# Optimization experiments

Measured on AMD Instinct MI355X. Metric: run time of the kernel, lower is better.

Reference implementation:

```python
import jax, jax.numpy as jnp
import numpy as np

# Dims (match init_kwargs / input_specs)
B, N, DIM, HEADS, DHEAD, CHUNK = 1, 2048, 1024, 8, 128, 64
HID = 4 * DHEAD            # MemoryMLP expansion_factor=4.0
DI = HEADS * DHEAD         # dim_inner
EPS = 1e-6
MAX_LR = 1.0               # default_step_transform_max_lr


def rmsnorm(x, w):
    return x * jax.lax.rsqrt(jnp.mean(jnp.square(x), -1, keepdims=True) + EPS) * w


def mem_forward(w0, w1, g, x):
    # ResidualNorm(MemoryMLP): y = RMSNorm(gelu(x@w0)@w1)*g + x
    h = jax.nn.gelu(x @ w0, approximate=False) @ w1
    return rmsnorm(h, g) + x


def setup_inputs() -> dict:
    key = jax.random.key(0)
    ks = jax.random.split(key, 12)
    s = lambda i, shape, sc: jax.random.normal(ks[i], shape, jnp.float32) * sc
    return dict(
        x=s(0, (B, N, DIM), 1.0),
        store_norm_w=jnp.ones((DIM,), jnp.float32),
        ret_norm_w=jnp.ones((DIM,), jnp.float32),
        Wq=s(1, (DIM, DI), DIM ** -0.5),
        Wk=s(2, (DIM, DI), DIM ** -0.5),
        Wv=s(3, (DIM, DI), DIM ** -0.5),
        W_step=s(4, (DIM, HEADS), DIM ** -0.5), b_step=jnp.zeros((HEADS,), jnp.float32),
        W_mom=s(5, (DIM, HEADS), DIM ** -0.5), b_mom=jnp.zeros((HEADS,), jnp.float32),
        W_decay=s(6, (DIM, HEADS), DIM ** -0.5), b_decay=jnp.zeros((HEADS,), jnp.float32),
        gate_W=s(7, (DIM, HEADS), DIM ** -0.5),
        combine_W=s(8, (DI, DIM), DI ** -0.5),
        mem_w0=s(9, (HEADS, DHEAD, HID), DHEAD ** -0.5),
        mem_w1=s(10, (HEADS, HID, DHEAD), HID ** -0.5),
        mem_g=jnp.ones((HEADS, DHEAD), jnp.float32),
    )


def reference(x, store_norm_w, ret_norm_w, Wq, Wk, Wv, W_step, b_step,
              W_mom, b_mom, W_decay, b_decay, gate_W, combine_W,
              mem_w0, mem_w1, mem_g):
    b, n, _ = x.shape
    nc = n // CHUNK
    BH = b * HEADS

    # ---- store path ----
    s = rmsnorm(x, store_norm_w)                                 # b n dim
    lr = jax.nn.sigmoid(s @ W_step + b_step) * MAX_LR            # b n h (per-token adaptive step)
    pooled = s.reshape(b, nc, CHUNK, DIM).mean(2)                # b nc dim (AveragePool chunk rep)
    mom = jax.nn.sigmoid(pooled @ W_mom + b_mom)                 # b nc h
    dec = jax.nn.sigmoid(pooled @ W_decay + b_decay)             # b nc h

    def to_chunks(t):  # b n (h d) -> (b h) nc c d
        return t.reshape(b, nc, CHUNK, HEADS, DHEAD).transpose(0, 3, 1, 2, 4).reshape(BH, nc, CHUNK, DHEAD)

    k = to_chunks(s @ Wk)
    v = to_chunks(s @ Wv)
    lr_c = lr.reshape(b, nc, CHUNK, HEADS).transpose(0, 3, 1, 2).reshape(BH, nc, CHUNK)
    mom_bh = mom.transpose(0, 2, 1).reshape(BH, nc)
    dec_bh = dec.transpose(0, 2, 1).reshape(BH, nc)

    # init fast weights per (b h)  (per_head_learned_parameters=True)
    w0 = jnp.broadcast_to(mem_w0[None], (b, HEADS, DHEAD, HID)).reshape(BH, DHEAD, HID)
    w1 = jnp.broadcast_to(mem_w1[None], (b, HEADS, HID, DHEAD)).reshape(BH, HID, DHEAD)
    g = jnp.broadcast_to(mem_g[None], (b, HEADS, DHEAD)).reshape(BH, DHEAD)

    def chunk_loss(w0_, w1_, g_, kc, vc, lrc):
        pred = mem_forward(w0_, w1_, g_, kc)                     # c d
        return jnp.sum(jnp.mean(jnp.square(pred - vc), -1) * lrc)

    grad_chunk = jax.grad(chunk_loss, argnums=(0, 1, 2))
    # vmap over chunks (same weights per chunk, per-sample grads), then over (b h)
    grads = jax.vmap(jax.vmap(grad_chunk, in_axes=(None, None, None, 0, 0, 0)))(w0, w1, g, k, v, lr_c)
    surprises = tuple(-gr for gr in grads)                       # each (BH, nc, ...)

    def combine(a, c):
        ga, xa = a
        gb, xb = c
        return (ga * gb, gb * xa + xb)

    def lin_scan(gates, xs):
        # y_i = gates_i * y_{i-1} + xs_i over chunk axis (axis=1)
        return jax.lax.associative_scan(combine, (gates, xs), axis=1)

    def expand(gates, ref):
        return gates.reshape(gates.shape + (1,) * (ref.ndim - 2))

    # momentum scan per parameter tensor
    updates = tuple(lin_scan(expand(mom_bh, su), su)[1] for su in surprises)

    # weight update scan: W_i = (1 - decay_i) * W_{i-1} + momentum_i, W_{-1} = init
    per_chunk_weights = []
    for upd, w_init in zip(updates, (w0, w1, g)):
        gates = expand(1.0 - dec_bh, upd)
        cumg, y = lin_scan(gates, upd)
        w_seq = y + cumg * w_init[:, None]                       # (BH, nc, ...)
        # retrieval at chunk i uses weights updated through chunk i-1
        per_chunk_weights.append(jnp.concatenate([w_init[:, None], w_seq[:, :-1]], axis=1))
    w0_c, w1_c, g_c = per_chunk_weights

    # ---- retrieve path ----
    r = rmsnorm(x, ret_norm_w)
    q = to_chunks(r @ Wq)                                        # (BH, nc, c, d)
    pred = jax.vmap(jax.vmap(mem_forward))(w0_c, w1_c, g_c, q)   # (BH, nc, c, d)
    out = pred.reshape(b, HEADS, n, DHEAD)                       # b h n d
    gate = jax.nn.sigmoid(r @ gate_W)                            # b n h (retrieve_gate, heads>1)
    out = out * gate.transpose(0, 2, 1)[..., None]
    out = out.transpose(0, 2, 1, 3).reshape(b, n, DI) @ combine_W
    return out
```

## Files before the change

kernel.cpp:

```cpp
#include <hip/hip_runtime.h>
#include <hip/hip_bf16.h>
#include <math.h>

#define NH   8
#define DHD  128
#define HIDN 512
#define CHK  64
#define NCH  32
#define MB   1048576ull

typedef unsigned short u16;
typedef unsigned int   u32;
typedef short s16x8 __attribute__((ext_vector_type(8)));
typedef float f32x4 __attribute__((ext_vector_type(4)));

#define MFMA(a,b,c) __builtin_amdgcn_mfma_f32_16x16x32_bf16((a),(b),(c),0,0,0)

__device__ __forceinline__ float bf2f(u16 v){ return __uint_as_float(((u32)v) << 16); }
__device__ __forceinline__ u16 f2bf(float f){
  u32 u = __float_as_uint(f);
  u += 0x7fffu + ((u >> 16) & 1u);
  return (u16)(u >> 16);
}
__device__ __forceinline__ u32 pack2(float a, float b){
  return (u32)f2bf(a) | ((u32)f2bf(b) << 16);
}
__device__ __forceinline__ float dot2(u32 a, u32 b){
  return __uint_as_float(a << 16)*__uint_as_float(b << 16)
       + __uint_as_float(a & 0xffff0000u)*__uint_as_float(b & 0xffff0000u);
}
__device__ __forceinline__ float waveRedSum(float v){
  #pragma unroll
  for (int off = 32; off; off >>= 1) v += __shfl_xor(v, off);
  return v;
}
__device__ __forceinline__ void gload16(const void* g, void* l){
  __builtin_amdgcn_global_load_lds(
      (const __attribute__((address_space(1))) u32*)g,
      (__attribute__((address_space(3))) u32*)l, 16, 0, 0);
}
__device__ __forceinline__ int swzb(int row, int colb){ return colb ^ ((row & 7) << 4); }
__device__ __forceinline__ int swza(int row, int colb){
  return colb ^ ((row & 7) << 4) ^ (((row >> 3) & 3) << 5);
}



__global__ __launch_bounds__(256) void k_rmsnorm(const float* __restrict__ x,
    const float* __restrict__ wst, const float* __restrict__ wrt,
    u16* __restrict__ s_bf, u16* __restrict__ r_bf){
  int row = blockIdx.x, t = threadIdx.x;
  float4 v = ((const float4*)(x + (size_t)row*1024))[t];
  float ss = v.x*v.x + v.y*v.y + v.z*v.z + v.w*v.w;
  ss = waveRedSum(ss);
  __shared__ float red[4];
  int wv = t >> 6, ln = t & 63;
  if (ln == 0) red[wv] = ss;
  __syncthreads();
  float rr = rsqrtf((red[0]+red[1]+red[2]+red[3])*(1.f/1024.f) + 1e-6f);
  float4 a = ((const float4*)wst)[t];
  float4 b = ((const float4*)wrt)[t];
  uint2 so = make_uint2(pack2(v.x*rr*a.x, v.y*rr*a.y), pack2(v.z*rr*a.z, v.w*rr*a.w));
  uint2 ro = make_uint2(pack2(v.x*rr*b.x, v.y*rr*b.y), pack2(v.z*rr*b.z, v.w*rr*b.w));
  *(uint2*)(s_bf + (size_t)row*1024 + t*4) = so;
  *(uint2*)(r_bf + (size_t)row*1024 + t*4) = ro;
}

__global__ __launch_bounds__(256) void k_pool(const u16* __restrict__ s_bf, float* __restrict__ pooled){
  int c = blockIdx.x; int d = blockIdx.y*256 + threadIdx.x;
  float acc = 0.f;
  for (int tt = 0; tt < 64; ++tt) acc += bf2f(s_bf[((size_t)c*64+tt)*1024 + d]);
  pooled[(size_t)c*1024 + d] = acc * (1.f/64.f);
}

__global__ __launch_bounds__(256) void k_lrgate(const u16* __restrict__ s_bf, const u16* __restrict__ r_bf,
    const u16* __restrict__ WsgL, const float* __restrict__ bstep,
    float* __restrict__ lrc, float* __restrict__ gate){
  int wv = threadIdx.x >> 6, ln = threadIdx.x & 63;
  int tok = blockIdx.x*4 + wv;
  const u16* sp = s_bf + (size_t)tok*1024 + ln*16;
  const u16* rp = r_bf + (size_t)tok*1024 + ln*16;
  uint4 s0 = *(const uint4*)sp, s1 = *(const uint4*)(sp+8);
  uint4 r0 = *(const uint4*)rp, r1 = *(const uint4*)(rp+8);
  #pragma unroll 4
  for (int o = 0; o < 16; ++o){
    const u16* wp = WsgL + (size_t)o*1024 + ln*16;
    uint4 w0v = *(const uint4*)wp, w1v = *(const uint4*)(wp+8);
    uint4 a0 = (o < 8) ? s0 : r0, a1 = (o < 8) ? s1 : r1;
    float acc = dot2(a0.x,w0v.x)+dot2(a0.y,w0v.y)+dot2(a0.z,w0v.z)+dot2(a0.w,w0v.w)
              + dot2(a1.x,w1v.x)+dot2(a1.y,w1v.y)+dot2(a1.z,w1v.z)+dot2(a1.w,w1v.w);
    acc = waveRedSum(acc);
    if (ln == 0){
      int h = o & 7;
      if (o < 8){
        float v = 1.f/(1.f+expf(-(acc + bstep[h])));
        lrc[((size_t)h*NCH + (tok>>6))*CHK + (tok&63)] = v;
      } else {
        gate[(size_t)tok*8 + h] = 1.f/(1.f+expf(-acc));
      }
    }
  }
}

__global__ __launch_bounds__(64) void k_momdec(const float* __restrict__ pooled,
    const float* __restrict__ Wmom, const float* __restrict__ bmom,
    const float* __restrict__ Wdec, const float* __restrict__ bdec,
    float* __restrict__ momb, float* __restrict__ decb){
  int c = blockIdx.x, ln = threadIdx.x;
  const float* prow = pooled + (size_t)c*1024;
  for (int o = 0; o < 16; ++o){
    int h = o & 7;
    const float* W = (o < 8) ? Wmom : Wdec;
    float acc = 0.f;
    for (int k = ln; k < 1024; k += 64) acc += prow[k]*W[(size_t)k*8+h];
    acc = waveRedSum(acc);
    if (ln == 0){
      float bb = (o < 8) ? bmom[h] : bdec[h];
      float v = 1.f/(1.f+expf(-(acc+bb)));
      if (o < 8) momb[h*NCH + c] = v; else decb[h*NCH + c] = v;
    }
  }
}

__global__ __launch_bounds__(256) void k_trf4(
    const float* __restrict__ A0, const float* __restrict__ A1,
    const float* __restrict__ A2, const float* __restrict__ A3,
    u16* __restrict__ O0, u16* __restrict__ O1, u16* __restrict__ O2, u16* __restrict__ O3){
  __shared__ u16 tile[32][34];
  int z = blockIdx.z;
  const float* in = (z==0)?A0:(z==1)?A1:(z==2)?A2:A3;
  u16* out = (z==0)?O0:(z==1)?O1:(z==2)?O2:O3;
  int c0 = blockIdx.x*32, r0 = blockIdx.y*32;
  int tx = threadIdx.x & 31, ty = threadIdx.x >> 5;
  #pragma unroll
  for (int k = 0; k < 4; ++k) tile[ty+k*8][tx] = f2bf(in[(size_t)(r0+ty+k*8)*1024 + c0+tx]);
  __syncthreads();
  #pragma unroll
  for (int k = 0; k < 4; ++k) out[(size_t)(c0+ty+k*8)*1024 + r0+tx] = tile[tx][ty+k*8];
}

__global__ __launch_bounds__(256) void k_packw(const float* __restrict__ mw0, const float* __restrict__ mw1,
    const float* __restrict__ Wstep, const float* __restrict__ gateW,
    u16* __restrict__ w0L, u16* __restrict__ w1L, u16* __restrict__ w1bL, u16* __restrict__ WsgL){
  int h = blockIdx.z, which = blockIdx.y;
  int i = blockIdx.x*256 + threadIdx.x;
  if (which == 3){
    if (h == 0 && i < 16384){
      int o = i >> 10, k = i & 1023;
      float v = (o < 8) ? Wstep[(size_t)k*8 + o] : gateW[(size_t)k*8 + (o-8)];
      WsgL[i] = f2bf(v);
    }
    return;
  }
  int r = i & 511, blk = i >> 9;
  int lg = r >> 7, lr = (r >> 3) & 15, e = r & 7;
  float v; u16* dst;
  if (which == 0){ int n0 = blk >> 2, ks = blk & 3; int hid = n0*16+lr, d = ks*32+lg*8+e;
    v = mw0[(size_t)h*65536 + (size_t)d*512 + hid]; dst = w0L; }
  else if (which == 1){ int n0 = blk >> 4, ks = blk & 15; int d = n0*16+lr, hid = ks*32+lg*8+e;
    v = mw1[(size_t)h*65536 + (size_t)hid*128 + d]; dst = w1L; }
  else { int n0 = blk >> 2, ks = blk & 3; int hid = n0*16+lr, d = ks*32+lg*8+e;
    v = mw1[(size_t)h*65536 + (size_t)hid*128 + d]; dst = w1bL; }
  dst[(size_t)h*65536 + i] = f2bf(v);
}

__device__ __forceinline__ void gemm_body(const u16* __restrict__ A, const u16* __restrict__ BT,
    void* __restrict__ Cp, int mode){
  __shared__ char As[8192];
  __shared__ char Bs[16384];
  int t = threadIdx.x, l = t & 63, w = t >> 6, lr16 = l & 15, lg = l >> 4;
  int wm = w & 1, wn = w >> 1;
  int bm = blockIdx.x*64, bn = blockIdx.y*128;
  f32x4 acc[2][2];
  #pragma unroll
  for (int mt = 0; mt < 2; ++mt)
    #pragma unroll
    for (int nt = 0; nt < 2; ++nt) acc[mt][nt] = (f32x4){0.f,0.f,0.f,0.f};
  for (int k0 = 0; k0 < 1024; k0 += 64){
    gload16(A  + (size_t)(bm + (t>>3))*1024      + k0 + (t&7)*8, As + w*1024);
    gload16(BT + (size_t)(bn + (t>>3))*1024      + k0 + (t&7)*8, Bs + w*1024);
    gload16(BT + (size_t)(bn + 64 + (t>>3))*1024 + k0 + (t&7)*8, Bs + 8192 + w*1024);
    __syncthreads();
    #pragma unroll
    for (int ks = 0; ks < 2; ++ks){
      s16x8 xa[2], yb[2];
      #pragma unroll
      for (int mt = 0; mt < 2; ++mt){ int row = wm*32 + mt*16 + lr16;
        xa[mt] = *(const s16x8*)(As + row*128 + ks*64 + lg*16); }
      #pragma unroll
      for (int nt = 0; nt < 2; ++nt){ int row = wn*32 + nt*16 + lr16;
        yb[nt] = *(const s16x8*)(Bs + row*128 + ks*64 + lg*16); }
      #pragma unroll
      for (int mt = 0; mt < 2; ++mt)
        #pragma unroll
        for (int nt = 0; nt < 2; ++nt) acc[mt][nt] = MFMA(xa[mt], yb[nt], acc[mt][nt]);
    }
    __syncthreads();
  }
  #pragma unroll
  for (int mt = 0; mt < 2; ++mt)
    #pragma unroll
    for (int nt = 0; nt < 2; ++nt)
      #pragma unroll
      for (int j = 0; j < 4; ++j){
        int row = bm + wm*32 + mt*16 + lg*4 + j;
        int coln = bn + wn*32 + nt*16 + lr16;
        if (mode == 0) ((float*)Cp)[(size_t)row*1024 + coln] = acc[mt][nt][j];
        else { int cI = row>>6, tok = row&63, h = coln>>7, d = coln&127;
          ((u16*)Cp)[((size_t)(h*32+cI)*64 + tok)*128 + d] = f2bf(acc[mt][nt][j]); }
      }
}

__global__ __launch_bounds__(512) void k_gemm_bf(const u16* __restrict__ A, const u16* __restrict__ BT,
    void* __restrict__ Cp, int mode){ gemm_body(A, BT, Cp, mode); }

__global__ __launch_bounds__(512) void k_gemm3(
    const u16* __restrict__ s_bf, const u16* __restrict__ r_bf,
    const u16* __restrict__ WkT, const u16* __restrict__ WvT, const u16* __restrict__ WqT,
    u16* __restrict__ Kc, u16* __restrict__ Vc, u16* __restrict__ Qc){
  int z = blockIdx.z;
  const u16* A = (z==2) ? r_bf : s_bf;
  const u16* BT = (z==0) ? WkT : (z==1) ? WvT : WqT;
  u16* C = (z==0) ? Kc : (z==1) ? Vc : Qc;
  gemm_body(A, BT, (void*)C, 1);
}

__global__ __launch_bounds__(512) void k_grad(
    const u16* __restrict__ Kc, const u16* __restrict__ Vc, const float* __restrict__ lrc,
    const u16* __restrict__ w0L, const u16* __restrict__ w1L, const u16* __restrict__ w1bL,
    const float* __restrict__ mg,
    u16* __restrict__ SW0, u16* __restrict__ SW1, float* __restrict__ SG){
  extern __shared__ char sm[];
  char* a_s   = sm;
  char* upT_s = sm + 65536;
  char* dh_s  = sm + 131072;
  char* dhT_s = sm + 147456;
  char* duT_s = a_s;
  char* kcT_s = upT_s;
  char* stg3  = dh_s;
  float* scr  = (float*)dh_s;

  int c = blockIdx.x, bh = blockIdx.y, t = threadIdx.x;
  size_t bc = (size_t)bh*NCH + c;
  int l = t & 63, w = t >> 6, lr16 = l & 15, lg = l >> 4;
  int tg = w & 3, dhf = w >> 2;
  int tokb = tg*16, tok0 = tokb + lg*4;

  const u16* kc_g = Kc + bc*8192;
  const u16* vc_g = Vc + bc*8192;

  s16x8 xk[4];
  #pragma unroll
  for (int k = 0; k < 4; ++k)
    xk[k] = *(const s16x8*)(kc_g + (size_t)(tokb+lr16)*128 + k*32 + lg*8);
  const u16* w0Lh = w0L + (size_t)bh*65536;
  for (int n0h = 0; n0h < 16; ++n0h){
    int n0 = dhf*16 + n0h;
    f32x4 acc = {0.f,0.f,0.f,0.f};
    const u16* yb = w0Lh + (size_t)n0*2048 + l*8;
    #pragma unroll
    for (int k = 0; k < 4; ++k) acc = MFMA(xk[k], *(const s16x8*)(yb + k*512), acc);
    int hid = n0*16 + lr16;
    float upv[4];
    #pragma unroll
    for (int j = 0; j < 4; ++j){
      int tok = tok0 + j;
      float u = acc[j];
      float cdf = 0.5f*(1.f + erff(u*0.70710678118654752f));
      upv[j] = cdf + u*0.3989422804014327f*expf(-0.5f*u*u);
      *(u16*)(a_s + tok*1024 + swza(tok, hid*2)) = f2bf(u*cdf);
    }
    *(uint2*)(upT_s + hid*128 + swzb(hid, tok0*2)) =
        make_uint2(pack2(upv[0], upv[1]), pack2(upv[2], upv[3]));
  }
  __syncthreads();

  s16x8 xa[16];
  #pragma unroll
  for (int k = 0; k < 16; ++k){ int row = tokb + lr16;
    xa[k] = *(const s16x8*)(a_s + row*1024 + swza(row, (k*32+lg*8)*2)); }
  const u16* w1Lh = w1L + (size_t)bh*65536;
  f32x4 hD[4];
  #pragma unroll
  for (int n0l = 0; n0l < 4; ++n0l){
    f32x4 acc = {0.f,0.f,0.f,0.f};
    const u16* yb = w1Lh + (size_t)(dhf*4 + n0l)*8192 + l*8;
    #pragma unroll
    for (int k = 0; k < 16; ++k) acc = MFMA(xa[k], *(const s16x8*)(yb + k*512), acc);
    hD[n0l] = acc;
  }
  #pragma unroll
  for (int j = 0; j < 4; ++j){
    float s = 0.f;
    #pragma unroll
    for (int n0l = 0; n0l < 4; ++n0l) s += hD[n0l][j]*hD[n0l][j];
    s += __shfl_xor(s,1); s += __shfl_xor(s,2); s += __shfl_xor(s,4); s += __shfl_xor(s,8);
    if (lr16 == 0) scr[dhf*64 + tok0 + j] = s;
  }
  __syncthreads();
  float rv[4], lrv[4], dotp[4];
  #pragma unroll
  for (int j = 0; j < 4; ++j){
    int tok = tok0 + j;
    float tot = scr[tok] + scr[64 + tok];
    rv[j] = rsqrtf(tot*(1.f/128.f) + 1e-6f);
    lrv[j] = lrc[bc*64 + tok];
    dotp[j] = 0.f;
  }
  float dn[4][4];
  #pragma unroll
  for (int n0l = 0; n0l < 4; ++n0l){
    int d = dhf*64 + n0l*16 + lr16;
    float g0 = mg[(size_t)bh*128 + d];
    float dgav = 0.f;
    #pragma unroll
    for (int j = 0; j < 4; ++j){
      int tok = tok0 + j;
      float h = hD[n0l][j];
      float nrm = h*rv[j];
      float kcv = bf2f(kc_g[(size_t)tok*128 + d]);
      float vcv = bf2f(vc_g[(size_t)tok*128 + d]);
      float p = nrm*g0 + kcv;
      float dp = (2.f/128.f)*lrv[j]*(p - vcv);
      dgav += dp*nrm;
      float dnv = dp*g0;
      dn[n0l][j] = dnv;
      dotp[j] += dnv*h;
    }
    dgav += __shfl_xor(dgav,16); dgav += __shfl_xor(dgav,32);
    if (lg == 0) scr[256 + w*64 + n0l*16 + lr16] = dgav;
  }
  #pragma unroll
  for (int j = 0; j < 4; ++j){
    float dd = dotp[j];
    dd += __shfl_xor(dd,1); dd += __shfl_xor(dd,2); dd += __shfl_xor(dd,4); dd += __shfl_xor(dd,8);
    if (lr16 == 0) scr[128 + dhf*64 + tok0 + j] = dd;
  }
  __syncthreads();
  float dotv[4];
  #pragma unroll
  for (int j = 0; j < 4; ++j){
    int tok = tok0 + j;
    dotv[j] = scr[128 + tok] + scr[128 + 64 + tok];
  }
  if (t < 128){
    int dh2 = t >> 6, dl = t & 63;
    float s = scr[256 + (dh2*4+0)*64 + dl] + scr[256 + (dh2*4+1)*64 + dl]
            + scr[256 + (dh2*4+2)*64 + dl] + scr[256 + (dh2*4+3)*64 + dl];
    SG[bc*128 + t] = -s;
  }
  __syncthreads();
  #pragma unroll
  for (int n0l = 0; n0l < 4; ++n0l){
    int d = dhf*64 + n0l*16 + lr16;
    float dhv[4];
    #pragma unroll
    for (int j = 0; j < 4; ++j){
      int tok = tok0 + j;
      float c3 = rv[j]*rv[j]*rv[j]*(1.f/128.f);
      dhv[j] = rv[j]*dn[n0l][j] - c3*dotv[j]*hD[n0l][j];
      *(u16*)(dh_s + tok*256 + swzb(tok, d*2)) = f2bf(dhv[j]);
    }
    *(uint2*)(dhT_s + d*128 + swzb(d, tok0*2)) =
        make_uint2(pack2(dhv[0], dhv[1]), pack2(dhv[2], dhv[3]));
  }
  __syncthreads();

  {
    s16x8 yB[4][2];
    #pragma unroll
    for (int n0l = 0; n0l < 4; ++n0l){
      int hid = w*64 + n0l*16 + lr16;
      #pragma unroll
      for (int ks = 0; ks < 2; ++ks){
        s16x8 v;
        #pragma unroll
        for (int e = 0; e < 8; ++e){ int tok = ks*32 + lg*8 + e;
          v[e] = *(const short*)(a_s + tok*1024 + swza(tok, hid*2)); }
        yB[n0l][ks] = v;
      }
    }
    __syncthreads();
    u16* stg = (u16*)(a_s + w*8192);
    #pragma unroll 1
    for (int half = 0; half < 2; ++half){
      #pragma unroll
      for (int mt4 = 0; mt4 < 4; ++mt4){
        int mt = half*4 + mt4; int row = mt*16 + lr16;
        s16x8 xD0 = *(const s16x8*)(dhT_s + row*128 + swzb(row, (lg*8)*2));
        s16x8 xD1 = *(const s16x8*)(dhT_s + row*128 + swzb(row, (32+lg*8)*2));
        #pragma unroll
        for (int n0l = 0; n0l < 4; ++n0l){
          f32x4 acc = {0.f,0.f,0.f,0.f};
          acc = MFMA(xD0, yB[n0l][0], acc);
          acc = MFMA(xD1, yB[n0l][1], acc);
          int base = mt4*1024 + (n0l>>1)*512 + (((n0l*2)+(lr16>>3))&3)*128 + (lr16&7);
          #pragma unroll
          for (int j = 0; j < 4; ++j)
            stg[base + (lg*4+j)*8] = f2bf(-acc[j]);
        }
      }
      asm volatile("s_waitcnt lgkmcnt(0)" ::: "memory");
      #pragma unroll
      for (int mt4 = 0; mt4 < 4; ++mt4){
        int mt = half*4 + mt4;
        u16* gb = SW1 + bc*65536 + (size_t)(mt*16 + w*2)*512;
        s16x8 o0 = *(const s16x8*)(stg + mt4*1024 + l*16);
        s16x8 o1 = *(const s16x8*)(stg + mt4*1024 + l*16 + 8);
        *(s16x8*)(gb + l*16) = o0;
        *(s16x8*)(gb + l*16 + 8) = o1;
      }
    }
  }
  __syncthreads();

  {
    s16x8 xDh[4][4];
    #pragma unroll
    for (int mt = 0; mt < 4; ++mt){ int row = mt*16 + lr16;
      #pragma unroll
      for (int ks = 0; ks < 4; ++ks)
        xDh[mt][ks] = *(const s16x8*)(dh_s + row*256 + swzb(row, (ks*32+lg*8)*2)); }
    const u16* w1bh = w1bL + (size_t)bh*65536;
    #pragma unroll 2
    for (int n0l = 0; n0l < 4; ++n0l){
      int hid = w*64 + n0l*16 + lr16;
      s16x8 yW[4];
      const u16* xb = w1bh + (size_t)(w*4 + n0l)*2048 + l*8;
      #pragma unroll
      for (int ks = 0; ks < 4; ++ks)
        yW[ks] = *(const s16x8*)(xb + ks*512);
      #pragma unroll
      for (int mt = 0; mt < 4; ++mt){
        f32x4 acc = {0.f,0.f,0.f,0.f};
        #pragma unroll
        for (int ks = 0; ks < 4; ++ks) acc = MFMA(xDh[mt][ks], yW[ks], acc);
        int tk0 = mt*16 + lg*4;
        uint2 ur = *(const uint2*)(upT_s + hid*128 + swzb(hid, tk0*2));
        float u0 = bf2f((u16)(ur.x & 0xffff)), u1 = bf2f((u16)(ur.x >> 16));
        float u2 = bf2f((u16)(ur.y & 0xffff)), u3 = bf2f((u16)(ur.y >> 16));
        *(uint2*)(duT_s + hid*128 + swzb(hid, tk0*2)) =
            make_uint2(pack2(acc[0]*u0, acc[1]*u1), pack2(acc[2]*u2, acc[3]*u3));
      }
    }
  }
  __syncthreads();

  #pragma unroll
  for (int i = 0; i < 2; ++i){
    int idx = i*512 + t;
    int tok = idx & 63, d0 = (idx >> 6)*8;
    s16x8 kv = *(const s16x8*)(kc_g + (size_t)tok*128 + d0);
    #pragma unroll
    for (int e = 0; e < 8; ++e)
      *(u16*)(kcT_s + (d0+e)*128 + swzb(d0+e, tok*2)) = kv[e];
  }
  __syncthreads();

  {
    s16x8 yK[8][2];
    #pragma unroll
    for (int n0 = 0; n0 < 8; ++n0){
      int d = n0*16 + lr16;
      #pragma unroll
      for (int ks = 0; ks < 2; ++ks)
        yK[n0][ks] = *(const s16x8*)(kcT_s + d*128 + swzb(d, (ks*32+lg*8)*2));
    }
    u16* stg = (u16*)(stg3 + w*4096);
    #pragma unroll 1
    for (int mi = 0; mi < 4; ++mi){
      int hid = w*64 + mi*16 + lr16;
      s16x8 xU0 = *(const s16x8*)(duT_s + hid*128 + swzb(hid, (lg*8)*2));
      s16x8 xU1 = *(const s16x8*)(duT_s + hid*128 + swzb(hid, (32+lg*8)*2));
      #pragma unroll
      for (int n0 = 0; n0 < 8; ++n0){
        f32x4 acc = {0.f,0.f,0.f,0.f};
        acc = MFMA(xU0, yK[n0][0], acc);
        acc = MFMA(xU1, yK[n0][1], acc);
        int base = (n0>>1)*512 + (((n0*2)+(lr16>>3))&3)*128 + (lr16&7);
        #pragma unroll
        for (int j = 0; j < 4; ++j)
          stg[base + (lg*4+j)*8] = f2bf(-acc[j]);
      }
      asm volatile("s_waitcnt lgkmcnt(0)" ::: "memory");
      u16* gb = SW0 + bc*65536 + (size_t)(w*4 + mi)*2048;
      #pragma unroll
      for (int q = 0; q < 4; ++q){
        s16x8 o = *(const s16x8*)(stg + l*32 + q*8);
        *(s16x8*)(gb + l*32 + q*8) = o;
      }
    }
  }
}

__global__ __launch_bounds__(256) void k_scan(
    const u16* __restrict__ w0L, const u16* __restrict__ w1L, const float* __restrict__ mg,
    const u16* __restrict__ SW0, const u16* __restrict__ SW1, const float* __restrict__ SG,
    const float* __restrict__ momb, const float* __restrict__ decb,
    u16* __restrict__ W0C, u16* __restrict__ W1C, float* __restrict__ GC){
  int bh = blockIdx.y;
  int e = blockIdx.x*256 + threadIdx.x;
  const float* momp = momb + bh*NCH;
  const float* decp = decb + bh*NCH;
  float m = 0.f, Wv;
  if (e < 65536){
    Wv = bf2f(w0L[(size_t)bh*65536 + e]);
    const u16* su = SW0 + (size_t)bh*NCH*65536 + e;
    u16* outp = W0C + (size_t)bh*NCH*65536 + e;
    for (int c = 0; c < NCH; ++c){
      outp[(size_t)c*65536] = f2bf(Wv);
      m = momp[c]*m + bf2f(su[(size_t)c*65536]);
      Wv = (1.f - decp[c])*Wv + m;
    }
  } else if (e < 131072){
    int e2 = e - 65536;
    Wv = bf2f(w1L[(size_t)bh*65536 + e2]);
    const u16* su = SW1 + (size_t)bh*NCH*65536 + e2;
    u16* outp = W1C + (size_t)bh*NCH*65536 + e2;
    for (int c = 0; c < NCH; ++c){
      outp[(size_t)c*65536] = f2bf(Wv);
      m = momp[c]*m + bf2f(su[(size_t)c*65536]);
      Wv = (1.f - decp[c])*Wv + m;
    }
  } else if (e < 131200){
    int e3 = e - 131072;
    Wv = mg[(size_t)bh*128 + e3];
    const float* su = SG + (size_t)bh*NCH*128 + e3;
    float* outp = GC + (size_t)bh*NCH*128 + e3;
    for (int c = 0; c < NCH; ++c){
      outp[(size_t)c*128] = Wv;
      m = momp[c]*m + su[(size_t)c*128];
      Wv = (1.f - decp[c])*Wv + m;
    }
  }
}

__global__ __launch_bounds__(512) void k_retr(
    const u16* __restrict__ Qc, const u16* __restrict__ W0C, const u16* __restrict__ W1C,
    const float* __restrict__ GC, const float* __restrict__ gate, u16* __restrict__ OH){
  extern __shared__ char sm[];
  char* a_s = sm;
  float* scr = (float*)(sm + 65536);
// ... 59 lines not shown
    int d = dhf*64 + n0l*16 + lr16;
    float g0 = GC[bc*128 + d];
    #pragma unroll
    for (int j = 0; j < 4; ++j){
      int tok = tg*16 + lg*4 + j; int tokg = c*64 + tok;
      float qv = bf2f(q_g[(size_t)tok*128 + d]);
      float p = hD[n0l][j]*rv[j]*g0 + qv;
      OH[(size_t)tokg*1024 + bh*128 + d] = f2bf(p*gtv[j]);
    }
  }
}

extern "C" void kernel_launch(void* const* d_in, const int* in_sizes, int n_in,
                              void* d_out, int out_size, void* d_ws, size_t ws_size,
                              hipStream_t stream) {
  (void)in_sizes; (void)n_in; (void)out_size; (void)ws_size;
  const float* x     = (const float*)d_in[0];
  const float* snw   = (const float*)d_in[1];
  const float* rnw   = (const float*)d_in[2];
  const float* Wq    = (const float*)d_in[3];
  const float* Wk    = (const float*)d_in[4];
  const float* Wv    = (const float*)d_in[5];
  const float* Wstep = (const float*)d_in[6];
  const float* bstep = (const float*)d_in[7];
  const float* Wmom  = (const float*)d_in[8];
  const float* bmom  = (const float*)d_in[9];
  const float* Wdec  = (const float*)d_in[10];
  const float* bdec  = (const float*)d_in[11];
  const float* gateW = (const float*)d_in[12];
  const float* combW = (const float*)d_in[13];
  const float* mw0   = (const float*)d_in[14];
  const float* mw1   = (const float*)d_in[15];
  const float* mg    = (const float*)d_in[16];
  float* out = (float*)d_out;

  char* Wb = (char*)d_ws;
  u16* Qc    = (u16*)(Wb + 0*MB);
  u16* Kc    = (u16*)(Wb + 4*MB);
  u16* Vc    = (u16*)(Wb + 8*MB);
  u16* s_bf  = (u16*)(Wb + 12*MB);
  u16* r_bf  = (u16*)(Wb + 16*MB);
  u16* WqT   = (u16*)(Wb + 20*MB);
  u16* WkT   = (u16*)(Wb + 22*MB);
  u16* WvT   = (u16*)(Wb + 24*MB);
  u16* combT = (u16*)(Wb + 26*MB);
  u16* w0L   = (u16*)(Wb + 28*MB);
  u16* w1L   = (u16*)(Wb + 29*MB);
  u16* w1bL  = (u16*)(Wb + 30*MB);
  u16* OH    = (u16*)(Wb + 31*MB);
  u16* SW0   = (u16*)(Wb + 35*MB);
  u16* SW1   = (u16*)(Wb + 67*MB);
  u16* W0C   = (u16*)(Wb + 99*MB);
  u16* W1C   = (u16*)(Wb + 131*MB);
  float* pooled = (float*)(Wb + 163*MB);
  float* lrc    = (float*)(Wb + 163*MB + 131072);
  float* momb   = (float*)(Wb + 163*MB + 196608);
  float* decb   = (float*)(Wb + 163*MB + 197632);
  float* gate   = (float*)(Wb + 163*MB + 198656);
  float* SG     = (float*)(Wb + 163*MB + 264192);
  float* GC     = (float*)(Wb + 163*MB + 395264);
  u16* WsgL  = (u16*)(Wb + 163*MB + 526336);

  hipFuncSetAttribute((const void*)k_grad, hipFuncAttributeMaxDynamicSharedMemorySize, 163840);
  hipFuncSetAttribute((const void*)k_retr, hipFuncAttributeMaxDynamicSharedMemorySize, 66560);

  k_rmsnorm<<<2048, 256, 0, stream>>>(x, snw, rnw, s_bf, r_bf);
  k_pool<<<dim3(32,4), 256, 0, stream>>>(s_bf, pooled);
  k_packw<<<dim3(256,4,8), 256, 0, stream>>>(mw0, mw1, Wstep, gateW, w0L, w1L, w1bL, WsgL);
  k_lrgate<<<512, 256, 0, stream>>>(s_bf, r_bf, WsgL, bstep, lrc, gate);
  k_momdec<<<32, 64, 0, stream>>>(pooled, Wmom, bmom, Wdec, bdec, momb, decb);
  k_trf4<<<dim3(32,32,4), 256, 0, stream>>>(Wq, Wk, Wv, combW, WqT, WkT, WvT, combT);
  k_gemm3<<<dim3(32,8,3), 512, 0, stream>>>(s_bf, r_bf, WkT, WvT, WqT, Kc, Vc, Qc);
  k_grad<<<dim3(32,8), 512, 163840, stream>>>(Kc, Vc, lrc, w0L, w1L, w1bL, mg, SW0, SW1, SG);
  k_scan<<<dim3(513,8), 256, 0, stream>>>(w0L, w1L, mg, SW0, SW1, SG, momb, decb, W0C, W1C, GC);
  k_retr<<<dim3(32,8), 512, 66560, stream>>>(Qc, W0C, W1C, GC, gate, OH);
  k_gemm_bf<<<dim3(32,8), 512, 0, stream>>>(OH, combT, (void*)out, 0);
}
```

Baseline: 228.3 us.

## Cut k_grad LDS to 80KB by keeping gelu' in registers and spilling dh to global

The LDS footprint of k_grad drops from 160KB to 80KB. The gelu-derivative tile moves from shared memory into per-thread registers, which means the first matmul's work split across waves changes. The dh tile is written to a global scratch buffer instead of LDS, and the staging area is reused within duT_s. Launch bounds request 4 waves per SIMD, with the aim of fitting two blocks per CU and overlapping their latency. The cost is extra global traffic for dh, possible register pressure, and a grid of only 256 blocks.

```diff
diff --git a/kernel.cpp b/kernel.cpp
--- a/kernel.cpp
+++ b/kernel.cpp
@@ -225,60 +225,57 @@
   gemm_body(A, BT, (void*)C, 1);
 }
 
-__global__ __launch_bounds__(512) void k_grad(
+__global__ __launch_bounds__(512, 4) void k_grad(
     const u16* __restrict__ Kc, const u16* __restrict__ Vc, const float* __restrict__ lrc,
     const u16* __restrict__ w0L, const u16* __restrict__ w1L, const u16* __restrict__ w1bL,
     const float* __restrict__ mg,
-    u16* __restrict__ SW0, u16* __restrict__ SW1, float* __restrict__ SG){
+    u16* __restrict__ SW0, u16* __restrict__ SW1, float* __restrict__ SG, u16* __restrict__ dhg){
   extern __shared__ char sm[];
   char* a_s   = sm;
-  char* upT_s = sm + 65536;
-  char* dh_s  = sm + 131072;
-  char* dhT_s = sm + 147456;
+  char* dhT_s = sm + 65536;
   char* duT_s = a_s;
-  char* kcT_s = upT_s;
-  char* stg3  = dh_s;
-  float* scr  = (float*)dh_s;
+  char* kcT_s = dhT_s;
+  float* scr  = (float*)dhT_s;
 
   int c = blockIdx.x, bh = blockIdx.y, t = threadIdx.x;
   size_t bc = (size_t)bh*NCH + c;
   int l = t & 63, w = t >> 6, lr16 = l & 15, lg = l >> 4;
+
+  const u16* kc_g = Kc + bc*8192;
+  const u16* vc_g = Vc + bc*8192;
+
+  uint2 upr[16];
+  const u16* w0Lh = w0L + (size_t)bh*65536;
+  #pragma unroll
+  for (int tgi = 0; tgi < 4; ++tgi){
+    s16x8 xk[4];
+    #pragma unroll
+    for (int ks = 0; ks < 4; ++ks)
+      xk[ks] = *(const s16x8*)(kc_g + (size_t)(tgi*16+lr16)*128 + ks*32 + lg*8);
+    #pragma unroll
+    for (int n0l = 0; n0l < 4; ++n0l){
+      int n0 = w*4 + n0l;
+      f32x4 acc = {0.f,0.f,0.f,0.f};
+      const u16* yb = w0Lh + (size_t)n0*2048 + l*8;
+      #pragma unroll
+      for (int ks = 0; ks < 4; ++ks) acc = MFMA(xk[ks], *(const s16x8*)(yb + ks*512), acc);
+      int hid = n0*16 + lr16;
+      float upv[4];
+      #pragma unroll
+      for (int j = 0; j < 4; ++j){
+        int tok = tgi*16 + lg*4 + j;
+        float u = acc[j];
+        float cdf = 0.5f*(1.f + erff(u*0.70710678118654752f));
+        upv[j] = cdf + u*0.3989422804014327f*expf(-0.5f*u*u);
+        *(u16*)(a_s + tok*1024 + swza(tok, hid*2)) = f2bf(u*cdf);
+      }
+      upr[tgi*4 + n0l] = make_uint2(pack2(upv[0], upv[1]), pack2(upv[2], upv[3]));
+    }
+  }
+  __syncthreads();
+
   int tg = w & 3, dhf = w >> 2;
   int tokb = tg*16, tok0 = tokb + lg*4;
-
-  const u16* kc_g = Kc + bc*8192;
-  const u16* vc_g = Vc + bc*8192;
-
-  s16x8 xk[4];
-  #pragma unroll
-  for (int k = 0; k < 4; ++k)
-    xk[k] = *(const s16x8*)(kc_g + (size_t)(tokb+lr16)*128 + k*32 + lg*8);
-  const u16* w0Lh = w0L + (size_t)bh*65536;
-  for (int n0h = 0; n0h < 16; ++n0h){
-    int n0 = dhf*16 + n0h;
-    f32x4 acc = {0.f,0.f,0.f,0.f};
-    const u16* yb = w0Lh + (size_t)n0*2048 + l*8;
-    #pragma unroll
-    for (int k = 0; k < 4; ++k) acc = MFMA(xk[k], *(const s16x8*)(yb + k*512), acc);
-    int hid = n0*16 + lr16;
-    float upv[4];
-    #pragma unroll
-    for (int j = 0; j < 4; ++j){
-      int tok = tok0 + j;
-      float u = acc[j];
-      float cdf = 0.5f*(1.f + erff(u*0.70710678118654752f));
-      upv[j] = cdf + u*0.3989422804014327f*expf(-0.5f*u*u);
-      *(u16*)(a_s + tok*1024 + swza(tok, hid*2)) = f2bf(u*cdf);
-    }
-    *(uint2*)(upT_s + hid*128 + swzb(hid, tok0*2)) =
-        make_uint2(pack2(upv[0], upv[1]), pack2(upv[2], upv[3]));
-  }
-  __syncthreads();
-
-  s16x8 xa[16];
-  #pragma unroll
-  for (int k = 0; k < 16; ++k){ int row = tokb + lr16;
-    xa[k] = *(const s16x8*)(a_s + row*1024 + swza(row, (k*32+lg*8)*2)); }
   const u16* w1Lh = w1L + (size_t)bh*65536;
   f32x4 hD[4];
   #pragma unroll
@@ -286,7 +283,16 @@
     f32x4 acc = {0.f,0.f,0.f,0.f};
     const u16* yb = w1Lh + (size_t)(dhf*4 + n0l)*8192 + l*8;
     #pragma unroll
-    for (int k = 0; k < 16; ++k) acc = MFMA(xa[k], *(const s16x8*)(yb + k*512), acc);
+    for (int kb = 0; kb < 4; ++kb){
+      s16x8 xa[4];
+      #pragma unroll
+      for (int kk = 0; kk < 4; ++kk){
+        int k = kb*4 + kk, row = tokb + lr16;
+        xa[kk] = *(const s16x8*)(a_s + row*1024 + swza(row, (k*32+lg*8)*2));
+      }
+      #pragma unroll
+      for (int kk = 0; kk < 4; ++kk) acc = MFMA(xa[kk], *(const s16x8*)(yb + (kb*4+kk)*512), acc);
+    }
     hD[n0l] = acc;
   }
   #pragma unroll
@@ -359,7 +365,7 @@
       int tok = tok0 + j;
       float c3 = rv[j]*rv[j]*rv[j]*(1.f/128.f);
       dhv[j] = rv[j]*dn[n0l][j] - c3*dotv[j]*hD[n0l][j];
-      *(u16*)(dh_s + tok*256 + swzb(tok, d*2)) = f2bf(dhv[j]);
+      dhg[bc*8192 + (size_t)tok*128 + d] = f2bf(dhv[j]);
     }
     *(uint2*)(dhT_s + d*128 + swzb(d, tok0*2)) =
         make_uint2(pack2(dhv[0], dhv[1]), pack2(dhv[2], dhv[3]));
@@ -414,29 +420,33 @@
   }
   __syncthreads();
 
+  #pragma unroll
+  for (int i = 0; i < 2; ++i){
+    int idx = i*512 + t;
+    int tok = idx & 63, d0 = (idx >> 6)*8;
+    s16x8 kv = *(const s16x8*)(kc_g + (size_t)tok*128 + d0);
+    #pragma unroll
+    for (int e = 0; e < 8; ++e)
+      *(u16*)(kcT_s + (d0+e)*128 + swzb(d0+e, tok*2)) = kv[e];
+  }
   {
-    s16x8 xDh[4][4];
-    #pragma unroll
-    for (int mt = 0; mt < 4; ++mt){ int row = mt*16 + lr16;
+    const u16* dhb = dhg + bc*8192;
+    const u16* w1bh = w1bL + (size_t)bh*65536;
+    #pragma unroll 1
+    for (int mt = 0; mt < 4; ++mt){
+      s16x8 xDh[4];
       #pragma unroll
       for (int ks = 0; ks < 4; ++ks)
-        xDh[mt][ks] = *(const s16x8*)(dh_s + row*256 + swzb(row, (ks*32+lg*8)*2)); }
-    const u16* w1bh = w1bL + (size_t)bh*65536;
-    #pragma unroll 2
-    for (int n0l = 0; n0l < 4; ++n0l){
-      int hid = w*64 + n0l*16 + lr16;
-      s16x8 yW[4];
-      const u16* xb = w1bh + (size_t)(w*4 + n0l)*2048 + l*8;
-      #pragma unroll
-      for (int ks = 0; ks < 4; ++ks)
-        yW[ks] = *(const s16x8*)(xb + ks*512);
-      #pragma unroll
-      for (int mt = 0; mt < 4; ++mt){
+        xDh[ks] = *(const s16x8*)(dhb + (size_t)(mt*16+lr16)*128 + ks*32 + lg*8);
+      #pragma unroll
+      for (int n0l = 0; n0l < 4; ++n0l){
+        int hid = w*64 + n0l*16 + lr16;
+        const u16* xb = w1bh + (size_t)(w*4 + n0l)*2048 + l*8;
         f32x4 acc = {0.f,0.f,0.f,0.f};
         #pragma unroll
-        for (int ks = 0; ks < 4; ++ks) acc = MFMA(xDh[mt][ks], yW[ks], acc);
+        for (int ks = 0; ks < 4; ++ks) acc = MFMA(xDh[ks], *(const s16x8*)(xb + ks*512), acc);
         int tk0 = mt*16 + lg*4;
-        uint2 ur = *(const uint2*)(upT_s + hid*128 + swzb(hid, tk0*2));
+        uint2 ur = upr[mt*4 + n0l];
         float u0 = bf2f((u16)(ur.x & 0xffff)), u1 = bf2f((u16)(ur.x >> 16));
         float u2 = bf2f((u16)(ur.y & 0xffff)), u3 = bf2f((u16)(ur.y >> 16));
         *(uint2*)(duT_s + hid*128 + swzb(hid, tk0*2)) =
@@ -446,17 +456,6 @@
   }
   __syncthreads();
 
-  #pragma unroll
-  for (int i = 0; i < 2; ++i){
-    int idx = i*512 + t;
-    int tok = idx & 63, d0 = (idx >> 6)*8;
-    s16x8 kv = *(const s16x8*)(kc_g + (size_t)tok*128 + d0);
-    #pragma unroll
-    for (int e = 0; e < 8; ++e)
-      *(u16*)(kcT_s + (d0+e)*128 + swzb(d0+e, tok*2)) = kv[e];
-  }
-  __syncthreads();
-
   {
     s16x8 yK[8][2];
     #pragma unroll
@@ -466,28 +465,31 @@
       for (int ks = 0; ks < 2; ++ks)
         yK[n0][ks] = *(const s16x8*)(kcT_s + d*128 + swzb(d, (ks*32+lg*8)*2));
     }
-    u16* stg = (u16*)(stg3 + w*4096);
     #pragma unroll 1
     for (int mi = 0; mi < 4; ++mi){
       int hid = w*64 + mi*16 + lr16;
       s16x8 xU0 = *(const s16x8*)(duT_s + hid*128 + swzb(hid, (lg*8)*2));
       s16x8 xU1 = *(const s16x8*)(duT_s + hid*128 + swzb(hid, (32+lg*8)*2));
-      #pragma unroll
-      for (int n0 = 0; n0 < 8; ++n0){
-        f32x4 acc = {0.f,0.f,0.f,0.f};
-        acc = MFMA(xU0, yK[n0][0], acc);
-        acc = MFMA(xU1, yK[n0][1], acc);
-        int base = (n0>>1)*512 + (((n0*2)+(lr16>>3))&3)*128 + (lr16&7);
+      u16* stgw = (u16*)(duT_s + (size_t)(w*64 + mi*16)*128);
+      u16* gb = SW0 + bc*65536 + (size_t)(w*4 + mi)*2048;
+      #pragma unroll 1
+      for (int hh = 0; hh < 2; ++hh){
         #pragma unroll
-        for (int j = 0; j < 4; ++j)
-          stg[base + (lg*4+j)*8] = f2bf(-acc[j]);
-      }
-      asm volatile("s_waitcnt lgkmcnt(0)" ::: "memory");
-      u16* gb = SW0 + bc*65536 + (size_t)(w*4 + mi)*2048;
-      #pragma unroll
-      for (int q = 0; q < 4; ++q){
-        s16x8 o = *(const s16x8*)(stg + l*32 + q*8);
-        *(s16x8*)(gb + l*32 + q*8) = o;
+        for (int n0h = 0; n0h < 4; ++n0h){
+          int n0 = hh*4 + n0h;
+          f32x4 acc = {0.f,0.f,0.f,0.f};
+          acc = MFMA(xU0, yK[n0][0], acc);
+          acc = MFMA(xU1, yK[n0][1], acc);
+          int base = (n0h>>1)*512 + (((n0*2)+(lr16>>3))&3)*128 + (lr16&7);
+          #pragma unroll
+          for (int j = 0; j < 4; ++j)
+            stgw[base + (lg*4+j)*8] = f2bf(-acc[j]);
+        }
+        asm volatile("s_waitcnt lgkmcnt(0)" ::: "memory");
+        s16x8 o0 = *(const s16x8*)(stgw + l*16);
+        s16x8 o1 = *(const s16x8*)(stgw + l*16 + 8);
+        *(s16x8*)(gb + hh*1024 + l*16) = o0;
+        *(s16x8*)(gb + hh*1024 + l*16 + 8) = o1;
       }
     }
   }
@@ -661,8 +663,9 @@
   float* SG     = (float*)(Wb + 163*MB + 264192);
   float* GC     = (float*)(Wb + 163*MB + 395264);
   u16* WsgL  = (u16*)(Wb + 163*MB + 526336);
-
-  hipFuncSetAttribute((const void*)k_grad, hipFuncAttributeMaxDynamicSharedMemorySize, 163840);
+  u16* dhg   = (u16*)(Wb + 164*MB);
+
+  hipFuncSetAttribute((const void*)k_grad, hipFuncAttributeMaxDynamicSharedMemorySize, 81920);
   hipFuncSetAttribute((const void*)k_retr, hipFuncAttributeMaxDynamicSharedMemorySize, 66560);
 
   k_rmsnorm<<<2048, 256, 0, stream>>>(x, snw, rnw, s_bf, r_bf);
@@ -672,7 +675,7 @@
   k_momdec<<<32, 64, 0, stream>>>(pooled, Wmom, bmom, Wdec, bdec, momb, decb);
   k_trf4<<<dim3(32,32,4), 256, 0, stream>>>(Wq, Wk, Wv, combW, WqT, WkT, WvT, combT);
   k_gemm3<<<dim3(32,8,3), 512, 0, stream>>>(s_bf, r_bf, WkT, WvT, WqT, Kc, Vc, Qc);
-  k_grad<<<dim3(32,8), 512, 163840, stream>>>(Kc, Vc, lrc, w0L, w1L, w1bL, mg, SW0, SW1, SG);
+  k_grad<<<dim3(32,8), 512, 81920, stream>>>(Kc, Vc, lrc, w0L, w1L, w1bL, mg, SW0, SW1, SG, dhg);
   k_scan<<<dim3(513,8), 256, 0, stream>>>(w0L, w1L, mg, SW0, SW1, SG, momb, decb, W0C, W1C, GC);
   k_retr<<<dim3(32,8), 512, 66560, stream>>>(Qc, W0C, W1C, GC, gate, OH);
   k_gemm_bf<<<dim3(32,8), 512, 0, stream>>>(OH, combT, (void*)out, 0);
```

Measured after the change: 259.7 us. 1.14x slower.

## Merge prep kernels, fuse pool with mom/decay, reorder grad blocks and staging

Applied to the files above, without the earlier changes.

Folds the weight transposes, memory-weight packing and step/gate weight packing into one k_prep launch. Merges pooling, momentum/decay projection and the lr/gate projection into a single k_lrmd launch, with pooled values held in LDS. This removes several launches and the pooled global buffer. k_grad now uses a 1D grid that puts the 8 heads of each chunk next to each other, and its final staging writes into the dead duT region in two halves instead of a separate stg3 buffer. The intent is lower launch overhead and less LDS pressure, at the cost of extra branches and serialized pooling within a block.

```diff
diff --git a/kernel.cpp b/kernel.cpp
--- a/kernel.cpp
+++ b/kernel.cpp
@@ -45,6 +45,50 @@
 }
 
 
+__global__ __launch_bounds__(256) void k_prep(
+    const float* __restrict__ Wq, const float* __restrict__ Wk,
+    const float* __restrict__ Wv, const float* __restrict__ combW,
+    const float* __restrict__ mw0, const float* __restrict__ mw1,
+    const float* __restrict__ Wstep, const float* __restrict__ gateW,
+    u16* __restrict__ WqT, u16* __restrict__ WkT, u16* __restrict__ WvT, u16* __restrict__ combT,
+    u16* __restrict__ w0L, u16* __restrict__ w1L, u16* __restrict__ w1bL, u16* __restrict__ WsgL){
+  __shared__ u16 tile[32][34];
+  int bid = blockIdx.x, t = threadIdx.x;
+  if (bid < 4096){
+    int z = bid >> 10, rem = bid & 1023;
+    const float* in = (z==0)?Wq:(z==1)?Wk:(z==2)?Wv:combW;
+    u16* out = (z==0)?WqT:(z==1)?WkT:(z==2)?WvT:combT;
+    int c0 = (rem & 31)*32, r0 = (rem >> 5)*32;
+    int tx = t & 31, ty = t >> 5;
+    #pragma unroll
+    for (int k = 0; k < 4; ++k) tile[ty+k*8][tx] = f2bf(in[(size_t)(r0+ty+k*8)*1024 + c0+tx]);
+    __syncthreads();
+    #pragma unroll
+    for (int k = 0; k < 4; ++k) out[(size_t)(c0+ty+k*8)*1024 + r0+tx] = tile[tx][ty+k*8];
+  } else if (bid < 10240){
+    int b2 = bid - 4096;
+    int which = b2 >> 11;
+    int h = (b2 >> 8) & 7;
+    int i = (b2 & 255)*256 + t;
+    int r = i & 511, blk = i >> 9;
+    int lg = r >> 7, lr = (r >> 3) & 15, e = r & 7;
+    float v; u16* dst;
+    if (which == 0){ int n0 = blk >> 2, ks = blk & 3; int hid = n0*16+lr, d = ks*32+lg*8+e;
+      v = mw0[(size_t)h*65536 + (size_t)d*512 + hid]; dst = w0L; }
+    else if (which == 1){ int n0 = blk >> 4, ks = blk & 15; int d = n0*16+lr, hid = ks*32+lg*8+e;
+      v = mw1[(size_t)h*65536 + (size_t)hid*128 + d]; dst = w1L; }
+    else { int n0 = blk >> 2, ks = blk & 3; int hid = n0*16+lr, d = ks*32+lg*8+e;
+      v = mw1[(size_t)h*65536 + (size_t)hid*128 + d]; dst = w1bL; }
+    dst[(size_t)h*65536 + i] = f2bf(v);
+  } else {
+    int i = (bid - 10240)*256 + t;
+    if (i < 16384){
+      int o = i >> 10, k = i & 1023;
+      float v = (o < 8) ? Wstep[(size_t)k*8 + o] : gateW[(size_t)k*8 + (o-8)];
+      WsgL[i] = f2bf(v);
+    }
+  }
+}
 
 __global__ __launch_bounds__(256) void k_rmsnorm(const float* __restrict__ x,
     const float* __restrict__ wst, const float* __restrict__ wrt,
@@ -66,102 +110,65 @@
   *(uint2*)(r_bf + (size_t)row*1024 + t*4) = ro;
 }
 
-__global__ __launch_bounds__(256) void k_pool(const u16* __restrict__ s_bf, float* __restrict__ pooled){
-  int c = blockIdx.x; int d = blockIdx.y*256 + threadIdx.x;
-  float acc = 0.f;
-  for (int tt = 0; tt < 64; ++tt) acc += bf2f(s_bf[((size_t)c*64+tt)*1024 + d]);
-  pooled[(size_t)c*1024 + d] = acc * (1.f/64.f);
-}
-
-__global__ __launch_bounds__(256) void k_lrgate(const u16* __restrict__ s_bf, const u16* __restrict__ r_bf,
+__global__ __launch_bounds__(256) void k_lrmd(const u16* __restrict__ s_bf, const u16* __restrict__ r_bf,
     const u16* __restrict__ WsgL, const float* __restrict__ bstep,
-    float* __restrict__ lrc, float* __restrict__ gate){
-  int wv = threadIdx.x >> 6, ln = threadIdx.x & 63;
-  int tok = blockIdx.x*4 + wv;
-  const u16* sp = s_bf + (size_t)tok*1024 + ln*16;
-  const u16* rp = r_bf + (size_t)tok*1024 + ln*16;
-  uint4 s0 = *(const uint4*)sp, s1 = *(const uint4*)(sp+8);
-  uint4 r0 = *(const uint4*)rp, r1 = *(const uint4*)(rp+8);
-  #pragma unroll 4
-  for (int o = 0; o < 16; ++o){
-    const u16* wp = WsgL + (size_t)o*1024 + ln*16;
-    uint4 w0v = *(const uint4*)wp, w1v = *(const uint4*)(wp+8);
-    uint4 a0 = (o < 8) ? s0 : r0, a1 = (o < 8) ? s1 : r1;
-    float acc = dot2(a0.x,w0v.x)+dot2(a0.y,w0v.y)+dot2(a0.z,w0v.z)+dot2(a0.w,w0v.w)
-              + dot2(a1.x,w1v.x)+dot2(a1.y,w1v.y)+dot2(a1.z,w1v.z)+dot2(a1.w,w1v.w);
-    acc = waveRedSum(acc);
-    if (ln == 0){
-      int h = o & 7;
-      if (o < 8){
-        float v = 1.f/(1.f+expf(-(acc + bstep[h])));
-        lrc[((size_t)h*NCH + (tok>>6))*CHK + (tok&63)] = v;
-      } else {
-        gate[(size_t)tok*8 + h] = 1.f/(1.f+expf(-acc));
-      }
-    }
-  }
-}
-
-__global__ __launch_bounds__(64) void k_momdec(const float* __restrict__ pooled,
     const float* __restrict__ Wmom, const float* __restrict__ bmom,
     const float* __restrict__ Wdec, const float* __restrict__ bdec,
+    float* __restrict__ lrc, float* __restrict__ gate,
     float* __restrict__ momb, float* __restrict__ decb){
-  int c = blockIdx.x, ln = threadIdx.x;
-  const float* prow = pooled + (size_t)c*1024;
-  for (int o = 0; o < 16; ++o){
-    int h = o & 7;
-    const float* W = (o < 8) ? Wmom : Wdec;
-    float acc = 0.f;
-    for (int k = ln; k < 1024; k += 64) acc += prow[k]*W[(size_t)k*8+h];
-    acc = waveRedSum(acc);
-    if (ln == 0){
-      float bb = (o < 8) ? bmom[h] : bdec[h];
-      float v = 1.f/(1.f+expf(-(acc+bb)));
-      if (o < 8) momb[h*NCH + c] = v; else decb[h*NCH + c] = v;
-    }
-  }
-}
-
-__global__ __launch_bounds__(256) void k_trf4(
-    const float* __restrict__ A0, const float* __restrict__ A1,
-    const float* __restrict__ A2, const float* __restrict__ A3,
-    u16* __restrict__ O0, u16* __restrict__ O1, u16* __restrict__ O2, u16* __restrict__ O3){
-  __shared__ u16 tile[32][34];
-  int z = blockIdx.z;
-  const float* in = (z==0)?A0:(z==1)?A1:(z==2)?A2:A3;
-  u16* out = (z==0)?O0:(z==1)?O1:(z==2)?O2:O3;
-  int c0 = blockIdx.x*32, r0 = blockIdx.y*32;
-  int tx = threadIdx.x & 31, ty = threadIdx.x >> 5;
-  #pragma unroll
-  for (int k = 0; k < 4; ++k) tile[ty+k*8][tx] = f2bf(in[(size_t)(r0+ty+k*8)*1024 + c0+tx]);
-  __syncthreads();
-  #pragma unroll
-  for (int k = 0; k < 4; ++k) out[(size_t)(c0+ty+k*8)*1024 + r0+tx] = tile[tx][ty+k*8];
-}
-
-__global__ __launch_bounds__(256) void k_packw(const float* __restrict__ mw0, const float* __restrict__ mw1,
-    const float* __restrict__ Wstep, const float* __restrict__ gateW,
-    u16* __restrict__ w0L, u16* __restrict__ w1L, u16* __restrict__ w1bL, u16* __restrict__ WsgL){
-  int h = blockIdx.z, which = blockIdx.y;
-  int i = blockIdx.x*256 + threadIdx.x;
-  if (which == 3){
-    if (h == 0 && i < 16384){
-      int o = i >> 10, k = i & 1023;
-      float v = (o < 8) ? Wstep[(size_t)k*8 + o] : gateW[(size_t)k*8 + (o-8)];
-      WsgL[i] = f2bf(v);
-    }
-    return;
-  }
-  int r = i & 511, blk = i >> 9;
-  int lg = r >> 7, lr = (r >> 3) & 15, e = r & 7;
-  float v; u16* dst;
-  if (which == 0){ int n0 = blk >> 2, ks = blk & 3; int hid = n0*16+lr, d = ks*32+lg*8+e;
-    v = mw0[(size_t)h*65536 + (size_t)d*512 + hid]; dst = w0L; }
-  else if (which == 1){ int n0 = blk >> 4, ks = blk & 15; int d = n0*16+lr, hid = ks*32+lg*8+e;
-    v = mw1[(size_t)h*65536 + (size_t)hid*128 + d]; dst = w1L; }
-  else { int n0 = blk >> 2, ks = blk & 3; int hid = n0*16+lr, d = ks*32+lg*8+e;
-    v = mw1[(size_t)h*65536 + (size_t)hid*128 + d]; dst = w1bL; }
-  dst[(size_t)h*65536 + i] = f2bf(v);
+  int bx = blockIdx.x;
+  if (bx < 512){
+    int wv = threadIdx.x >> 6, ln = threadIdx.x & 63;
+    int tok = bx*4 + wv;
+    const u16* sp = s_bf + (size_t)tok*1024 + ln*16;
+    const u16* rp = r_bf + (size_t)tok*1024 + ln*16;
+    uint4 s0 = *(const uint4*)sp, s1 = *(const uint4*)(sp+8);
+    uint4 r0 = *(const uint4*)rp, r1 = *(const uint4*)(rp+8);
+    #pragma unroll 4
+    for (int o = 0; o < 16; ++o){
+      const u16* wp = WsgL + (size_t)o*1024 + ln*16;
+      uint4 w0v = *(const uint4*)wp, w1v = *(const uint4*)(wp+8);
+      uint4 a0 = (o < 8) ? s0 : r0, a1 = (o < 8) ? s1 : r1;
+      float acc = dot2(a0.x,w0v.x)+dot2(a0.y,w0v.y)+dot2(a0.z,w0v.z)+dot2(a0.w,w0v.w)
+                + dot2(a1.x,w1v.x)+dot2(a1.y,w1v.y)+dot2(a1.z,w1v.z)+dot2(a1.w,w1v.w);
+      acc = waveRedSum(acc);
+      if (ln == 0){
+        int h = o & 7;
+        if (o < 8){
+          float v = 1.f/(1.f+expf(-(acc + bstep[h])));
+          lrc[((size_t)h*NCH + (tok>>6))*CHK + (tok&63)] = v;
+        } else {
+          gate[(size_t)tok*8 + h] = 1.f/(1.f+expf(-acc));
+        }
+      }
+    }
+  } else {
+    __shared__ float plds[1024];
+    int c = bx - 512, t = threadIdx.x;
+    #pragma unroll
+    for (int q = 0; q < 4; ++q){
+      int d = q*256 + t;
+      float acc = 0.f;
+      for (int tt = 0; tt < 64; ++tt) acc += bf2f(s_bf[((size_t)c*64+tt)*1024 + d]);
+      plds[d] = acc * (1.f/64.f);
+    }
+    __syncthreads();
+    if (t < 64){
+      int ln = t;
+      for (int o = 0; o < 16; ++o){
+        int h = o & 7;
+        const float* W = (o < 8) ? Wmom : Wdec;
+        float acc = 0.f;
+        for (int k = ln; k < 1024; k += 64) acc += plds[k]*W[(size_t)k*8+h];
+        acc = waveRedSum(acc);
+        if (ln == 0){
+          float bb = (o < 8) ? bmom[h] : bdec[h];
+          float v = 1.f/(1.f+expf(-(acc+bb)));
+          if (o < 8) momb[h*NCH + c] = v; else decb[h*NCH + c] = v;
+        }
+      }
+    }
+  }
 }
 
 __device__ __forceinline__ void gemm_body(const u16* __restrict__ A, const u16* __restrict__ BT,
@@ -237,10 +244,11 @@
   char* dhT_s = sm + 147456;
   char* duT_s = a_s;
   char* kcT_s = upT_s;
-  char* stg3  = dh_s;
   float* scr  = (float*)dh_s;
 
-  int c = blockIdx.x, bh = blockIdx.y, t = threadIdx.x;
+  int bid = blockIdx.x;
+  int c = bid >> 3, bh = bid & 7;
+  int t = threadIdx.x;
   size_t bc = (size_t)bh*NCH + c;
   int l = t & 63, w = t >> 6, lr16 = l & 15, lg = l >> 4;
   int tg = w & 3, dhf = w >> 2;
@@ -466,28 +474,31 @@
       for (int ks = 0; ks < 2; ++ks)
         yK[n0][ks] = *(const s16x8*)(kcT_s + d*128 + swzb(d, (ks*32+lg*8)*2));
     }
-    u16* stg = (u16*)(stg3 + w*4096);
     #pragma unroll 1
     for (int mi = 0; mi < 4; ++mi){
       int hid = w*64 + mi*16 + lr16;
       s16x8 xU0 = *(const s16x8*)(duT_s + hid*128 + swzb(hid, (lg*8)*2));
       s16x8 xU1 = *(const s16x8*)(duT_s + hid*128 + swzb(hid, (32+lg*8)*2));
-      #pragma unroll
-      for (int n0 = 0; n0 < 8; ++n0){
-        f32x4 acc = {0.f,0.f,0.f,0.f};
-        acc = MFMA(xU0, yK[n0][0], acc);
-        acc = MFMA(xU1, yK[n0][1], acc);
-        int base = (n0>>1)*512 + (((n0*2)+(lr16>>3))&3)*128 + (lr16&7);
+      u16* stgw = (u16*)(duT_s + (size_t)(w*64 + mi*16)*128);
+      u16* gb = SW0 + bc*65536 + (size_t)(w*4 + mi)*2048;
+      #pragma unroll 1
+      for (int hh = 0; hh < 2; ++hh){
         #pragma unroll
-        for (int j = 0; j < 4; ++j)
-          stg[base + (lg*4+j)*8] = f2bf(-acc[j]);
-      }
-      asm volatile("s_waitcnt lgkmcnt(0)" ::: "memory");
-      u16* gb = SW0 + bc*65536 + (size_t)(w*4 + mi)*2048;
-      #pragma unroll
-      for (int q = 0; q < 4; ++q){
-        s16x8 o = *(const s16x8*)(stg + l*32 + q*8);
-        *(s16x8*)(gb + l*32 + q*8) = o;
+        for (int n0h = 0; n0h < 4; ++n0h){
+          int n0 = hh*4 + n0h;
+          f32x4 acc = {0.f,0.f,0.f,0.f};
+          acc = MFMA(xU0, yK[n0][0], acc);
+          acc = MFMA(xU1, yK[n0][1], acc);
+          int base = (n0h>>1)*512 + (((n0h*2)+(lr16>>3))&3)*128 + (lr16&7);
+          #pragma unroll
+          for (int j = 0; j < 4; ++j)
+            stgw[base + (lg*4+j)*8] = f2bf(-acc[j]);
+        }
+        asm volatile("s_waitcnt lgkmcnt(0)" ::: "memory");
+        s16x8 o0 = *(const s16x8*)(stgw + l*16);
+        s16x8 o1 = *(const s16x8*)(stgw + l*16 + 8);
+        *(s16x8*)(gb + hh*1024 + l*16) = o0;
+        *(s16x8*)(gb + hh*1024 + l*16 + 8) = o1;
       }
     }
   }
@@ -653,7 +664,6 @@
   u16* SW1   = (u16*)(Wb + 67*MB);
   u16* W0C   = (u16*)(Wb + 99*MB);
   u16* W1C   = (u16*)(Wb + 131*MB);
-  float* pooled = (float*)(Wb + 163*MB);
   float* lrc    = (float*)(Wb + 163*MB + 131072);
   float* momb   = (float*)(Wb + 163*MB + 196608);
   float* decb   = (float*)(Wb + 163*MB + 197632);
@@ -665,14 +675,13 @@
   hipFuncSetAttribute((const void*)k_grad, hipFuncAttributeMaxDynamicSharedMemorySize, 163840);
   hipFuncSetAttribute((const void*)k_retr, hipFuncAttributeMaxDynamicSharedMemorySize, 66560);
 
+  k_prep<<<10304, 256, 0, stream>>>(Wq, Wk, Wv, combW, mw0, mw1, Wstep, gateW,
+                                    WqT, WkT, WvT, combT, w0L, w1L, w1bL, WsgL);
   k_rmsnorm<<<2048, 256, 0, stream>>>(x, snw, rnw, s_bf, r_bf);
-  k_pool<<<dim3(32,4), 256, 0, stream>>>(s_bf, pooled);
-  k_packw<<<dim3(256,4,8), 256, 0, stream>>>(mw0, mw1, Wstep, gateW, w0L, w1L, w1bL, WsgL);
-  k_lrgate<<<512, 256, 0, stream>>>(s_bf, r_bf, WsgL, bstep, lrc, gate);
-  k_momdec<<<32, 64, 0, stream>>>(pooled, Wmom, bmom, Wdec, bdec, momb, decb);
-  k_trf4<<<dim3(32,32,4), 256, 0, stream>>>(Wq, Wk, Wv, combW, WqT, WkT, WvT, combT);
+  k_lrmd<<<544, 256, 0, stream>>>(s_bf, r_bf, WsgL, bstep, Wmom, bmom, Wdec, bdec,
+                                  lrc, gate, momb, decb);
   k_gemm3<<<dim3(32,8,3), 512, 0, stream>>>(s_bf, r_bf, WkT, WvT, WqT, Kc, Vc, Qc);
-  k_grad<<<dim3(32,8), 512, 163840, stream>>>(Kc, Vc, lrc, w0L, w1L, w1bL, mg, SW0, SW1, SG);
+  k_grad<<<256, 512, 163840, stream>>>(Kc, Vc, lrc, w0L, w1L, w1bL, mg, SW0, SW1, SG);
   k_scan<<<dim3(513,8), 256, 0, stream>>>(w0L, w1L, mg, SW0, SW1, SG, momb, decb, W0C, W1C, GC);
   k_retr<<<dim3(32,8), 512, 66560, stream>>>(Qc, W0C, W1C, GC, gate, OH);
   k_gemm_bf<<<dim3(32,8), 512, 0, stream>>>(OH, combT, (void*)out, 0);
```

After: 232.4 us. Within noise of the previous version (+1.8%).
